# Performance work log

Measured on AMD Instinct MI355X. Metric: run time of the kernel, lower is better.

Reference implementation:

```python
import jax, jax.numpy as jnp
import numpy as np

EMBED_DIM = 512
NUM_HEADS = 8
HEAD_DIM = EMBED_DIM // NUM_HEADS
FACTOR = 5
B, T = 4, 2048


def setup_inputs() -> dict:
    key = jax.random.key(0)
    ks = jax.random.split(key, 10)
    s = EMBED_DIM ** -0.5
    hidden_states = jax.random.normal(ks[0], (B, T, EMBED_DIM), dtype=jnp.float32)
    log_L = int(np.ceil(np.log1p(T)))
    u_part = min(FACTOR * T * log_L, T)
    index_sample = jax.random.randint(ks[1], (u_part,), 0, T, dtype=jnp.int32)
    Wq = jax.random.normal(ks[2], (EMBED_DIM, EMBED_DIM), dtype=jnp.float32) * s
    bq = jnp.zeros((EMBED_DIM,), dtype=jnp.float32)
    Wk = jax.random.normal(ks[3], (EMBED_DIM, EMBED_DIM), dtype=jnp.float32) * s
    bk = jnp.zeros((EMBED_DIM,), dtype=jnp.float32)
    Wv = jax.random.normal(ks[4], (EMBED_DIM, EMBED_DIM), dtype=jnp.float32) * s
    bv = jnp.zeros((EMBED_DIM,), dtype=jnp.float32)
    Wo = jax.random.normal(ks[5], (EMBED_DIM, EMBED_DIM), dtype=jnp.float32) * s
    bo = jnp.zeros((EMBED_DIM,), dtype=jnp.float32)
    return {"hidden_states": hidden_states, "index_sample": index_sample,
            "Wq": Wq, "bq": bq, "Wk": Wk, "bk": bk, "Wv": Wv, "bv": bv,
            "Wo": Wo, "bo": bo}


def _split_heads(x, bsz, seqlen):
    # [B, T, E] -> [B*H, T, head_dim]
    return x.reshape(bsz, seqlen, NUM_HEADS, HEAD_DIM).transpose(0, 2, 1, 3).reshape(bsz * NUM_HEADS, seqlen, HEAD_DIM)


def reference(hidden_states, index_sample, Wq, bq, Wk, bk, Wv, bv, Wo, bo):
    bsz, tgt_len, embed_dim = hidden_states.shape
    scaling = HEAD_DIM ** -0.5
    q = (hidden_states @ Wq.T + bq) * scaling
    k = hidden_states @ Wk.T + bk
    v = hidden_states @ Wv.T + bv
    q = _split_heads(q, bsz, tgt_len)   # [BH, T, d]
    k = _split_heads(k, bsz, tgt_len)
    v = _split_heads(v, bsz, tgt_len)
    L_k = tgt_len
    log_q = int(np.ceil(np.log1p(tgt_len)))
    u = min(FACTOR * log_q, tgt_len)
    # random key sampling (indices precomputed, length u_part)
    k_sample = k[:, index_sample, :]                                  # [BH, u_part, d]
    qk_sample = jnp.einsum('bqd,bkd->bqk', q, k_sample)               # [BH, T, u_part]
    # sparsity measurement: max - mean over sampled keys (mean uses full L_k as in source)
    sparsity = qk_sample.max(axis=-1) - qk_sample.sum(axis=-1) / L_k  # [BH, T]
    top_idx = jax.lax.top_k(sparsity, u)[1]                           # [BH, u]
    q_reduce = jnp.take_along_axis(q, top_idx[:, :, None], axis=1)    # [BH, u, d]
    attn = jax.nn.softmax(jnp.einsum('bud,bkd->buk', q_reduce, k), axis=-1)  # [BH, u, L]
    attn_out = jnp.einsum('buk,bkd->bud', attn, v)                    # [BH, u, d]
    # encoder context: mean of values over time, scattered with active-query outputs
    context = jnp.broadcast_to(v.mean(axis=1, keepdims=True), v.shape)  # [BH, T, d]
    bh_idx = jnp.arange(bsz * NUM_HEADS)[:, None]
    context = context.at[bh_idx, top_idx].set(attn_out)
    out = context.reshape(bsz, NUM_HEADS, tgt_len, HEAD_DIM).transpose(0, 2, 1, 3).reshape(bsz, tgt_len, embed_dim)
    return out @ Wo.T + bo
```

## Files before the change

### kernel.cpp

```cpp
#include <hip/hip_runtime.h>
#include <hip/hip_bf16.h>
#include <math.h>

#define T_LEN 2048
#define EMB   512
#define NHEAD 8
#define HDIM  64
#define BHEADS 32
#define USEL  40

typedef __bf16 bf16v8 __attribute__((ext_vector_type(8)));
typedef _Float16 f16x8 __attribute__((ext_vector_type(8)));
typedef float f32x4 __attribute__((ext_vector_type(4)));
typedef unsigned short u16;

__device__ __forceinline__ void cvt4_hilo(const float4 f, uint2& ph, uint2& pl)
{
    __hip_bfloat16 h0 = __float2bfloat16(f.x);
    __hip_bfloat16 h1 = __float2bfloat16(f.y);
    __hip_bfloat16 h2 = __float2bfloat16(f.z);
    __hip_bfloat16 h3 = __float2bfloat16(f.w);
    __hip_bfloat16 l0 = __float2bfloat16(f.x - __bfloat162float(h0));
    __hip_bfloat16 l1 = __float2bfloat16(f.y - __bfloat162float(h1));
    __hip_bfloat16 l2 = __float2bfloat16(f.z - __bfloat162float(h2));
    __hip_bfloat16 l3 = __float2bfloat16(f.w - __bfloat162float(h3));
    ph.x = (unsigned)*(const u16*)&h0 | ((unsigned)*(const u16*)&h1 << 16);
    ph.y = (unsigned)*(const u16*)&h2 | ((unsigned)*(const u16*)&h3 << 16);
    pl.x = (unsigned)*(const u16*)&l0 | ((unsigned)*(const u16*)&l1 << 16);
    pl.y = (unsigned)*(const u16*)&l2 | ((unsigned)*(const u16*)&l3 << 16);
}

__device__ __forceinline__ void cvt4_hilo_h(const float4 f, uint2& ph, uint2& pl)
{
    _Float16 h0 = (_Float16)f.x;
    _Float16 h1 = (_Float16)f.y;
    _Float16 h2 = (_Float16)f.z;
    _Float16 h3 = (_Float16)f.w;
    _Float16 l0 = (_Float16)(f.x - (float)h0);
    _Float16 l1 = (_Float16)(f.y - (float)h1);
    _Float16 l2 = (_Float16)(f.z - (float)h2);
    _Float16 l3 = (_Float16)(f.w - (float)h3);
    ph.x = (unsigned)*(const u16*)&h0 | ((unsigned)*(const u16*)&h1 << 16);
    ph.y = (unsigned)*(const u16*)&h2 | ((unsigned)*(const u16*)&h3 << 16);
    pl.x = (unsigned)*(const u16*)&l0 | ((unsigned)*(const u16*)&l1 << 16);
    pl.y = (unsigned)*(const u16*)&l2 | ((unsigned)*(const u16*)&l3 << 16);
}

__global__ __launch_bounds__(256)
void pack_hilo_kernel(const float* __restrict__ X,
                      const float* __restrict__ Wq, const float* __restrict__ Wk,
                      const float* __restrict__ Wv,
                      u16* __restrict__ Xp, u16* __restrict__ Wp)
{
    alignas(16) __shared__ u16 th[4096];
    alignas(16) __shared__ u16 tl[4096];
    const int b = blockIdx.x, tid = threadIdx.x;

    const float* src; u16* dst;
    if (b < 1024) {
        int mt = b >> 4, kt = b & 15;
        src = X + (size_t)(mt * 128) * EMB + kt * 32;
        dst = Xp + (size_t)b * 8192;
    } else {
        int wdx = b - 1024;
        int z = wdx >> 6, nt = (wdx >> 4) & 3, kt = wdx & 15;
        const float* W = (z == 0) ? Wq : (z == 1) ? Wk : Wv;
        src = W + (size_t)(nt * 128) * EMB + kt * 32;
        dst = Wp + (size_t)wdx * 8192;
    }

    #pragma unroll
    for (int s = 0; s < 4; ++s) {
        int u = tid + 256 * s;
        int row = u >> 3, c4 = u & 7;
        float4 f = *(const float4*)&src[(size_t)row * EMB + c4 * 4];
        uint2 ph, pl;
        cvt4_hilo_h(f, ph, pl);
        int kq = c4 >> 1, e4 = (c4 & 1) * 4;
        *(uint2*)&th[kq * 1024 + row * 8 + e4] = ph;
        *(uint2*)&tl[kq * 1024 + row * 8 + e4] = pl;
    }
    __syncthreads();

    uint4* d4 = (uint4*)dst;
    const uint4* s4h = (const uint4*)th;
    const uint4* s4l = (const uint4*)tl;
    d4[tid]       = s4h[tid];
    d4[tid + 256] = s4h[tid + 256];
    d4[tid + 512] = s4l[tid];
    d4[tid + 768] = s4l[tid + 256];
}

__global__ __launch_bounds__(256)
void qkv_mfma_kernel(const u16* __restrict__ Xp, const u16* __restrict__ Wp,
                     const float* __restrict__ bq, const float* __restrict__ bk,
                     const float* __restrict__ bv,
                     float* __restrict__ qo, float* __restrict__ ko, float* __restrict__ vo)
{
    alignas(16) __shared__ u16 Ah[4096];
    alignas(16) __shared__ u16 Al[4096];
    alignas(16) __shared__ u16 Bh[4096];
    alignas(16) __shared__ u16 Bl[4096];

    const int z = blockIdx.z;
    const float* bias; float* dst; float scale;
    if (z == 0)      { bias = bq; dst = qo; scale = 0.125f; }
    else if (z == 1) { bias = bk; dst = ko; scale = 1.0f;   }
    else             { bias = bv; dst = vo; scale = 1.0f;   }
    const bool three = (z != 2);

    const int tid = threadIdx.x;
    const int mt = blockIdx.x;
    const int nt = blockIdx.y;
    const int w = tid >> 6, lane = tid & 63;
    const int wm = w & 1, wn = w >> 1;
    const int lm = lane & 15, kq = lane >> 4;

    const u16* Abase = Xp + (size_t)mt * (16 * 8192);
    const u16* Bbase = Wp + (size_t)(z * 4 + nt) * (16 * 8192);

    f32x4 acc[4][4];
    #pragma unroll
    for (int i = 0; i < 4; ++i)
        #pragma unroll
        for (int j = 0; j < 4; ++j)
            #pragma unroll
            for (int r = 0; r < 4; ++r) acc[i][j][r] = 0.0f;

    for (int kt = 0; kt < 16; ++kt) {
        __syncthreads();
        const u16* at = Abase + kt * 8192;
        const u16* bt = Bbase + kt * 8192;
        const u16* gsrc; u16* ldst;
        if (w == 0)      { gsrc = at;        ldst = Ah; }
        else if (w == 1) { gsrc = at + 4096; ldst = Al; }
        else if (w == 2) { gsrc = bt;        ldst = Bh; }
        else             { gsrc = bt + 4096; ldst = Bl; }
        if (three || (w & 1) == 0) {
            #pragma unroll
            for (int i = 0; i < 8; ++i)
                __builtin_amdgcn_global_load_lds(
                    (const __attribute__((address_space(1))) void*)(gsrc + (size_t)lane * 8 + i * 512),
                    (__attribute__((address_space(3))) void*)(ldst + i * 512),
                    16, 0, 0);
        }
        __syncthreads();

        f16x8 ah[4], al[4], bh[4], bl[4];
        #pragma unroll
        for (int i = 0; i < 4; ++i) {
            int ar = (wm * 64 + i * 16 + lm) * 8 + kq * 1024;
            int br = (wn * 64 + i * 16 + lm) * 8 + kq * 1024;
            ah[i] = *(const f16x8*)&Ah[ar];
            bh[i] = *(const f16x8*)&Bh[br];
            if (three) {
                al[i] = *(const f16x8*)&Al[ar];
                bl[i] = *(const f16x8*)&Bl[br];
            }
        }
        #pragma unroll
        for (int i = 0; i < 4; ++i)
            #pragma unroll
            for (int j = 0; j < 4; ++j) {
                acc[i][j] = __builtin_amdgcn_mfma_f32_16x16x32_f16(ah[i], bh[j], acc[i][j], 0, 0, 0);
                if (three) {
                    acc[i][j] = __builtin_amdgcn_mfma_f32_16x16x32_f16(ah[i], bl[j], acc[i][j], 0, 0, 0);
                    acc[i][j] = __builtin_amdgcn_mfma_f32_16x16x32_f16(al[i], bh[j], acc[i][j], 0, 0, 0);
                }
            }
    }

    #pragma unroll
    for (int j = 0; j < 4; ++j) {
        int ng = nt * 128 + wn * 64 + j * 16 + lm;
        int h = ng >> 6, d = ng & 63;
        float bv_ = bias[ng];
        #pragma unroll
        for (int i = 0; i < 4; ++i) {
            #pragma unroll
            for (int r = 0; r < 4; ++r) {
                int mg = mt * 128 + wm * 64 + i * 16 + kq * 4 + r;
                int b = mg >> 11, t = mg & 2047;
                dst[((size_t)((b * NHEAD + h) * T_LEN + t)) * HDIM + d] =
                    (acc[i][j][r] + bv_) * scale;
            }
        }
    }
}

__global__ __launch_bounds__(256)
void qkv_proj_kernel(const float* __restrict__ X,
                     const float* __restrict__ Wq, const float* __restrict__ bq,
                     const float* __restrict__ Wk, const float* __restrict__ bk,
                     const float* __restrict__ Wv, const float* __restrict__ bv,
                     float* __restrict__ qo, float* __restrict__ ko, float* __restrict__ vo)
{
    alignas(16) __shared__ u16 Ah[128 * 40];
    alignas(16) __shared__ u16 Al[128 * 40];
    alignas(16) __shared__ u16 Bh[128 * 40];
    alignas(16) __shared__ u16 Bl[128 * 40];

    const int z = blockIdx.z;
    const float* W; const float* bias; float* dst; float scale;
    if (z == 0)      { W = Wq; bias = bq; dst = qo; scale = 0.125f; }
    else if (z == 1) { W = Wk; bias = bk; dst = ko; scale = 1.0f;   }
    else             { W = Wv; bias = bv; dst = vo; scale = 1.0f;   }

    const int tid = threadIdx.x;
    const int m0 = blockIdx.x * 128;
    const int n0 = blockIdx.y * 128;
    const int w = tid >> 6, lane = tid & 63;
    const int wm = w & 1, wn = w >> 1;
    const int lm = lane & 15, kq = lane >> 4;

    f32x4 acc[4][4];
    #pragma unroll
    for (int i = 0; i < 4; ++i)
        #pragma unroll
        for (int j = 0; j < 4; ++j)
            #pragma unroll
            for (int r = 0; r < 4; ++r) acc[i][j][r] = 0.0f;

    for (int kc = 0; kc < EMB; kc += 32) {
        __syncthreads();
        #pragma unroll
        for (int s = 0; s < 4; ++s) {
            int u = tid + 256 * s;
            int row = u >> 3, c4 = u & 7;
            float4 fa = *(const float4*)&X[(size_t)(m0 + row) * EMB + kc + c4 * 4];
            float4 fb = *(const float4*)&W[(n0 + row) * EMB + kc + c4 * 4];
            uint2 ph, pl;
            cvt4_hilo_h(fa, ph, pl);
            *(uint2*)&Ah[row * 40 + c4 * 4] = ph;
            *(uint2*)&Al[row * 40 + c4 * 4] = pl;
            cvt4_hilo_h(fb, ph, pl);
            *(uint2*)&Bh[row * 40 + c4 * 4] = ph;
            *(uint2*)&Bl[row * 40 + c4 * 4] = pl;
        }
        __syncthreads();

        f16x8 ah[4], al[4], bh[4], bl[4];
        #pragma unroll
        for (int i = 0; i < 4; ++i) {
            int ra = (wm * 64 + i * 16 + lm) * 40 + kq * 8;
            ah[i] = *(const f16x8*)&Ah[ra];
            al[i] = *(const f16x8*)&Al[ra];
            int rb = (wn * 64 + i * 16 + lm) * 40 + kq * 8;
            bh[i] = *(const f16x8*)&Bh[rb];
            bl[i] = *(const f16x8*)&Bl[rb];
        }
        #pragma unroll
        for (int i = 0; i < 4; ++i)
            #pragma unroll
            for (int j = 0; j < 4; ++j) {
                acc[i][j] = __builtin_amdgcn_mfma_f32_16x16x32_f16(ah[i], bh[j], acc[i][j], 0, 0, 0);
                acc[i][j] = __builtin_amdgcn_mfma_f32_16x16x32_f16(ah[i], bl[j], acc[i][j], 0, 0, 0);
                acc[i][j] = __builtin_amdgcn_mfma_f32_16x16x32_f16(al[i], bh[j], acc[i][j], 0, 0, 0);
            }
    }

    #pragma unroll
    for (int j = 0; j < 4; ++j) {
        int ng = n0 + wn * 64 + j * 16 + lm;
        int h = ng >> 6, d = ng & 63;
        float bv_ = bias[ng];
        #pragma unroll
        for (int i = 0; i < 4; ++i) {
            #pragma unroll
            for (int r = 0; r < 4; ++r) {
                int mg = m0 + wm * 64 + i * 16 + kq * 4 + r;
                int b = mg >> 11, t = mg & 2047;
                dst[((size_t)((b * NHEAD + h) * T_LEN + t)) * HDIM + d] =
                    (acc[i][j][r] + bv_) * scale;
            }
        }
    }
}

__global__ __launch_bounds__(256)
void count_compact_kernel(const int* __restrict__ idxs, int n,
                          int* __restrict__ count, int* __restrict__ klist,
                          int* __restrict__ ncp)
{
    __shared__ int cnt[T_LEN];
    __shared__ int th_tot[256];
    __shared__ int th_off[256];
    __shared__ int ncs;
    const int tid = threadIdx.x;
    for (int j = tid; j < T_LEN; j += 256) cnt[j] = 0;
    __syncthreads();
    for (int i = tid; i < n; i += 256) atomicAdd(&cnt[idxs[i] & (T_LEN - 1)], 1);
    __syncthreads();
    const int base = tid * 8;
    int flags[8]; int loc = 0;
    #pragma unroll
    for (int j = 0; j < 8; ++j) {
        int c = cnt[base + j];
        count[base + j] = c;
        flags[j] = (c > 0); loc += flags[j];
    }
    th_tot[tid] = loc;
    __syncthreads();
    if (tid == 0) {
        int run = 0;
        for (int i = 0; i < 256; ++i) { th_off[i] = run; run += th_tot[i]; }
        ncs = run;
        ncp[0] = run;
    }
    __syncthreads();
    int off = th_off[tid];
    #pragma unroll
    for (int j = 0; j < 8; ++j)
        if (flags[j]) klist[off++] = base + j;
    __syncthreads();
    const int nc = ncs;
    const int nt = (nc + 127) & ~127;
    const int k0 = klist[0];
    for (int j = nc + tid; j < nt; j += 256) klist[j] = k0;
}

__global__ __launch_bounds__(256)
void ksum_vmean_part_kernel(const int* __restrict__ count,
                            const float* __restrict__ k, const float* __restrict__ v,
                            float* __restrict__ kpart, float* __restrict__ vpart)
{
    __shared__ int cs[256];
    alignas(16) __shared__ float rk[16 * 64];
    alignas(16) __shared__ float rv[16 * 64];

    const int sl = blockIdx.x, bh = blockIdx.y, tid = threadIdx.x;
    const int f4 = tid & 15, tg = tid >> 4;
    const int t0 = sl * 256;

    cs[tid] = count[t0 + tid];
    __syncthreads();

    const float4* k4 = (const float4*)(k + (size_t)bh * T_LEN * HDIM) + t0 * 16;
    const float4* v4 = (const float4*)(v + (size_t)bh * T_LEN * HDIM) + t0 * 16;

    float4 ak = {0.f, 0.f, 0.f, 0.f}, av = {0.f, 0.f, 0.f, 0.f};
    #pragma unroll
    for (int s = 0; s < 16; ++s) {
        int t = tg + s * 16;
        float c = (float)cs[t];
        float4 kf = k4[t * 16 + f4];
        float4 vf = v4[t * 16 + f4];
        ak.x = fmaf(c, kf.x, ak.x); ak.y = fmaf(c, kf.y, ak.y);
        ak.z = fmaf(c, kf.z, ak.z); ak.w = fmaf(c, kf.w, ak.w);
        av.x += vf.x; av.y += vf.y; av.z += vf.z; av.w += vf.w;
    }
    *(float4*)&rk[tg * 64 + f4 * 4] = ak;
    *(float4*)&rv[tg * 64 + f4 * 4] = av;
    __syncthreads();

    if (tid < 64) {
        float sk = 0.f, sv = 0.f;
        #pragma unroll
        for (int g = 0; g < 16; ++g) { sk += rk[g * 64 + tid]; sv += rv[g * 64 + tid]; }
        kpart[((size_t)bh * 8 + sl) * 64 + tid] = sk;
        vpart[((size_t)bh * 8 + sl) * 64 + tid] = sv;
    }
}

__global__ __launch_bounds__(64)
void ksum_vmean_reduce_kernel(const float* __restrict__ kpart, const float* __restrict__ vpart,
                              float* __restrict__ ksum, float* __restrict__ vmean)
{
    const int bh = blockIdx.x, d = threadIdx.x;
    float sk = 0.f, sv = 0.f;
    #pragma unroll
    for (int sl = 0; sl < 8; ++sl) {
        sk += kpart[((size_t)bh * 8 + sl) * 64 + d];
        sv += vpart[((size_t)bh * 8 + sl) * 64 + d];
    }
    ksum[bh * 64 + d]  = sk;
    vmean[bh * 64 + d] = sv * (1.0f / 2048.0f);
}

__global__ __launch_bounds__(256)
void pack_k_kernel(const float* __restrict__ k, const int* __restrict__ klist,
                   const int* __restrict__ ncp, u16* __restrict__ Kp)
{
    alignas(16) __shared__ u16 th[8192];
    alignas(16) __shared__ u16 tl[8192];
    const int wg = blockIdx.x, tid = threadIdx.x;
    const int swz = (wg & 7) * 64 + (wg >> 3);
    const int bh = swz >> 4, kt = swz & 15;
    const int ntiles = (ncp[0] + 127) >> 7;
    if (kt >= ntiles) return;

    const float4* kb4 = (const float4*)(k + (size_t)bh * T_LEN * HDIM);
    #pragma unroll
    for (int s = 0; s < 8; ++s) {
        int u = tid + 256 * s;
        int row = u >> 4, c4 = u & 15;
        int krow = klist[kt * 128 + row];
        float4 f = kb4[krow * 16 + c4];
        uint2 ph, pl;
        cvt4_hilo_h(f, ph, pl);
        int base = (c4 >> 3) * 4096 + ((c4 >> 1) & 3) * 1024 + row * 8 + (c4 & 1) * 4;
        *(uint2*)&th[base] = ph;
        *(uint2*)&tl[base] = pl;
    }
    __syncthreads();

    u16* dst = Kp + ((size_t)bh * 16 + kt) * 16384;
    uint4* d4 = (uint4*)dst;
    const uint4* s4h = (const uint4*)th;
    const uint4* s4l = (const uint4*)tl;
    #pragma unroll
    for (int i = 0; i < 4; ++i) d4[tid + 256 * i] = s4h[tid + 256 * i];
    #pragma unroll
    for (int i = 0; i < 4; ++i) d4[1024 + tid + 256 * i] = s4l[tid + 256 * i];
}

__global__ __launch_bounds__(256)
void sparsity_scan_kernel(const float* __restrict__ q, const u16* __restrict__ Kp,
                          const float* __restrict__ ksum,
                          const int* __restrict__ ncp, float* __restrict__ spars)
{
    alignas(16) __shared__ u16 KH[10240];
    alignas(16) __shared__ u16 KL[10240];
    __shared__ float ksm[64];
    __shared__ float smax[128];
    __shared__ float sdotL[128];

    const int tid = threadIdx.x;
    const int wg = blockIdx.x;
    const int swz = (wg & 7) * 64 + (wg >> 3);
    const int bh = swz >> 4;
    const int q0 = (swz & 15) * 128;
    const int w = tid >> 6, lane = tid & 63;
    const int lm = lane & 15, kq = lane >> 4;

    const float* qb = q + ((size_t)bh * T_LEN + q0) * HDIM;
    const int ntiles = (ncp[0] + 127) >> 7;

    if (tid < 64) ksm[tid] = ksum[bh * 64 + tid];

    #pragma unroll
    for (int s = 0; s < 8; ++s) {
        int u = tid + 256 * s;
        int row = u >> 4, c4 = u & 15;
        float4 f = *(const float4*)&qb[row * HDIM + c4 * 4];
        uint2 ph, pl;
        cvt4_hilo_h(f, ph, pl);
        int base = ((c4 >> 3) * 128 + row) * 40 + (c4 & 7) * 4;
        *(uint2*)&KH[base] = ph;
        *(uint2*)&KL[base] = pl;
    }
    __syncthreads();

    f16x8 qh[2][2], ql[2][2];
    #pragma unroll
    for (int i = 0; i < 2; ++i)
        #pragma unroll
        for (int c = 0; c < 2; ++c) {
            int ra = (c * 128 + w * 32 + i * 16 + lm) * 40 + kq * 8;
            qh[i][c] = *(const f16x8*)&KH[ra];
            ql[i][c] = *(const f16x8*)&KL[ra];
        }

    {
        float4 k0a = *(const float4*)&ksm[kq * 8];
        float4 k0b = *(const float4*)&ksm[kq * 8 + 4];
        float4 k1a = *(const float4*)&ksm[32 + kq * 8];
        float4 k1b = *(const float4*)&ksm[32 + kq * 8 + 4];
        float kmv[2][8] = {{k0a.x, k0a.y, k0a.z, k0a.w, k0b.x, k0b.y, k0b.z, k0b.w},
                           {k1a.x, k1a.y, k1a.z, k1a.w, k1b.x, k1b.y, k1b.z, k1b.w}};
        #pragma unroll
        for (int i = 0; i < 2; ++i) {
            float sd = 0.f;
            #pragma unroll
            for (int c = 0; c < 2; ++c)
                #pragma unroll
                for (int e = 0; e < 8; ++e)
                    sd = fmaf((float)qh[i][c][e] + (float)ql[i][c][e], kmv[c][e], sd);
            sd += __shfl_xor(sd, 16, 64);
            sd += __shfl_xor(sd, 32, 64);
            if (kq == 0) sdotL[w * 32 + i * 16 + lm] = sd;
        }
    }

    float vmax[2][4];
    #pragma unroll
    for (int i = 0; i < 2; ++i)
        #pragma unroll
        for (int r = 0; r < 4; ++r) vmax[i][r] = -INFINITY;

    const u16* kpb = Kp + (size_t)bh * (16 * 16384);

    for (int kt = 0; kt < ntiles; ++kt) {
        __syncthreads();
        const u16* kp = kpb + kt * 16384;
        const u16* gsrc; u16* ldst;
        if (w == 0)      { gsrc = kp;         ldst = KH; }
        else if (w == 1) { gsrc = kp + 4096;  ldst = KH + 4096; }
        else if (w == 2) { gsrc = kp + 8192;  ldst = KL; }
        else             { gsrc = kp + 12288; ldst = KL + 4096; }
        #pragma unroll
        for (int i = 0; i < 8; ++i)
            __builtin_amdgcn_global_load_lds(
                (const __attribute__((address_space(1))) void*)(gsrc + (size_t)lane * 8 + i * 512),
                (__attribute__((address_space(3))) void*)(ldst + i * 512),
                16, 0, 0);
        __syncthreads();

        #pragma unroll
        for (int j = 0; j < 8; ++j) {
            int rb0 = kq * 1024 + (j * 16 + lm) * 8;
            int rb1 = 4096 + kq * 1024 + (j * 16 + lm) * 8;
            f16x8 bh0 = *(const f16x8*)&KH[rb0];
            f16x8 bl0 = *(const f16x8*)&KL[rb0];
            f16x8 bh1 = *(const f16x8*)&KH[rb1];
            f16x8 bl1 = *(const f16x8*)&KL[rb1];
            f32x4 a0 = {0.f, 0.f, 0.f, 0.f};
            f32x4 a1 = {0.f, 0.f, 0.f, 0.f};
            a0 = __builtin_amdgcn_mfma_f32_16x16x32_f16(qh[0][0], bh0, a0, 0, 0, 0);
            a1 = __builtin_amdgcn_mfma_f32_16x16x32_f16(qh[1][0], bh0, a1, 0, 0, 0);
            a0 = __builtin_amdgcn_mfma_f32_16x16x32_f16(qh[0][0], bl0, a0, 0, 0, 0);
            a1 = __builtin_amdgcn_mfma_f32_16x16x32_f16(qh[1][0], bl0, a1, 0, 0, 0);
            a0 = __builtin_amdgcn_mfma_f32_16x16x32_f16(ql[0][0], bh0, a0, 0, 0, 0);
            a1 = __builtin_amdgcn_mfma_f32_16x16x32_f16(ql[1][0], bh0, a1, 0, 0, 0);
            a0 = __builtin_amdgcn_mfma_f32_16x16x32_f16(qh[0][1], bh1, a0, 0, 0, 0);
            a1 = __builtin_amdgcn_mfma_f32_16x16x32_f16(qh[1][1], bh1, a1, 0, 0, 0);
            a0 = __builtin_amdgcn_mfma_f32_16x16x32_f16(qh[0][1], bl1, a0, 0, 0, 0);
            a1 = __builtin_amdgcn_mfma_f32_16x16x32_f16(qh[1][1], bl1, a1, 0, 0, 0);
            a0 = __builtin_amdgcn_mfma_f32_16x16x32_f16(ql[0][1], bh1, a0, 0, 0, 0);
            a1 = __builtin_amdgcn_mfma_f32_16x16x32_f16(ql[1][1], bh1, a1, 0, 0, 0);
            #pragma unroll
            for (int r = 0; r < 4; ++r) {
                vmax[0][r] = fmaxf(vmax[0][r], a0[r]);
                vmax[1][r] = fmaxf(vmax[1][r], a1[r]);
            }
        }
    }

    #pragma unroll
    for (int i = 0; i < 2; ++i)
        #pragma unroll
        for (int r = 0; r < 4; ++r) {
            float m = vmax[i][r];
            m = fmaxf(m, __shfl_xor(m, 1, 64));
            m = fmaxf(m, __shfl_xor(m, 2, 64));
            m = fmaxf(m, __shfl_xor(m, 4, 64));
            m = fmaxf(m, __shfl_xor(m, 8, 64));
            if (lm == 0) smax[w * 32 + i * 16 + kq * 4 + r] = m;
        }
    __syncthreads();

    if (tid < 128)
        spars[bh * T_LEN + q0 + tid] = smax[tid] - sdotL[tid] * (1.0f / 2048.0f);
}

__global__ __launch_bounds__(256)
void sparsity_scan_fb_kernel(const float* __restrict__ q, const float* __restrict__ k,
                             const float* __restrict__ ksum, const int* __restrict__ klist,
                             const int* __restrict__ ncp, float* __restrict__ spars)
{
    alignas(16) __shared__ u16 KH[256 * 40];
    alignas(16) __shared__ u16 KL[256 * 40];
    __shared__ float ksm[64];
    __shared__ float smax[128];
    __shared__ float sdotL[128];

    const int tid = threadIdx.x;
    const int bh = blockIdx.y;
    const int q0 = blockIdx.x * 128;
    const int w = tid >> 6, lane = tid & 63;
    const int lm = lane & 15, kq = lane >> 4;

    const float* qb = q + ((size_t)bh * T_LEN + q0) * HDIM;
    const float4* kb4 = (const float4*)(k + (size_t)bh * T_LEN * HDIM);
    const int ntiles = (ncp[0] + 127) >> 7;

    if (tid < 64) ksm[tid] = ksum[bh * 64 + tid];

    #pragma unroll
    for (int s = 0; s < 8; ++s) {
        int u = tid + 256 * s;
        int row = u >> 4, c4 = u & 15;
        float4 f = *(const float4*)&qb[row * HDIM + c4 * 4];
        uint2 ph, pl;
        cvt4_hilo_h(f, ph, pl);
        int base = ((c4 >> 3) * 128 + row) * 40 + (c4 & 7) * 4;
        *(uint2*)&KH[base] = ph;
        *(uint2*)&KL[base] = pl;
    }
    __syncthreads();

    f16x8 qh[2][2], ql[2][2];
    #pragma unroll
    for (int i = 0; i < 2; ++i)
        #pragma unroll
        for (int c = 0; c < 2; ++c) {
            int ra = (c * 128 + w * 32 + i * 16 + lm) * 40 + kq * 8;
            qh[i][c] = *(const f16x8*)&KH[ra];
            ql[i][c] = *(const f16x8*)&KL[ra];
        }

    {
        float4 k0a = *(const float4*)&ksm[kq * 8];
        float4 k0b = *(const float4*)&ksm[kq * 8 + 4];
        float4 k1a = *(const float4*)&ksm[32 + kq * 8];
        float4 k1b = *(const float4*)&ksm[32 + kq * 8 + 4];
        float kmv[2][8] = {{k0a.x, k0a.y, k0a.z, k0a.w, k0b.x, k0b.y, k0b.z, k0b.w},
                           {k1a.x, k1a.y, k1a.z, k1a.w, k1b.x, k1b.y, k1b.z, k1b.w}};
        #pragma unroll
        for (int i = 0; i < 2; ++i) {
            float sd = 0.f;
            #pragma unroll
            for (int c = 0; c < 2; ++c)
                #pragma unroll
                for (int e = 0; e < 8; ++e)
                    sd = fmaf((float)qh[i][c][e] + (float)ql[i][c][e], kmv[c][e], sd);
            sd += __shfl_xor(sd, 16, 64);
            sd += __shfl_xor(sd, 32, 64);
            if (kq == 0) sdotL[w * 32 + i * 16 + lm] = sd;
        }
    }

    float vmax[2][4];
    #pragma unroll
    for (int i = 0; i < 2; ++i)
        #pragma unroll
        for (int r = 0; r < 4; ++r) vmax[i][r] = -INFINITY;

    for (int kt = 0; kt < ntiles; ++kt) {
        __syncthreads();
        #pragma unroll
        for (int s = 0; s < 8; ++s) {
            int u = tid + 256 * s;
            int row = u >> 4, c4 = u & 15;
            int krow = klist[kt * 128 + row];
            float4 f = kb4[krow * 16 + c4];
            uint2 ph, pl;
            cvt4_hilo_h(f, ph, pl);
            int base = ((c4 >> 3) * 128 + row) * 40 + (c4 & 7) * 4;
            *(uint2*)&KH[base] = ph;
            *(uint2*)&KL[base] = pl;
        }
        __syncthreads();

        #pragma unroll
        for (int j = 0; j < 8; ++j) {
            int rb0 = (j * 16 + lm) * 40 + kq * 8;
            int rb1 = (128 + j * 16 + lm) * 40 + kq * 8;
            f16x8 bh0 = *(const f16x8*)&KH[rb0];
            f16x8 bl0 = *(const f16x8*)&KL[rb0];
            f16x8 bh1 = *(const f16x8*)&KH[rb1];
            f16x8 bl1 = *(const f16x8*)&KL[rb1];
            f32x4 a0 = {0.f, 0.f, 0.f, 0.f};
            f32x4 a1 = {0.f, 0.f, 0.f, 0.f};
            a0 = __builtin_amdgcn_mfma_f32_16x16x32_f16(qh[0][0], bh0, a0, 0, 0, 0);
            a1 = __builtin_amdgcn_mfma_f32_16x16x32_f16(qh[1][0], bh0, a1, 0, 0, 0);
            a0 = __builtin_amdgcn_mfma_f32_16x16x32_f16(qh[0][0], bl0, a0, 0, 0, 0);
            a1 = __builtin_amdgcn_mfma_f32_16x16x32_f16(qh[1][0], bl0, a1, 0, 0, 0);
            a0 = __builtin_amdgcn_mfma_f32_16x16x32_f16(ql[0][0], bh0, a0, 0, 0, 0);
            a1 = __builtin_amdgcn_mfma_f32_16x16x32_f16(ql[1][0], bh0, a1, 0, 0, 0);
            a0 = __builtin_amdgcn_mfma_f32_16x16x32_f16(qh[0][1], bh1, a0, 0, 0, 0);
            a1 = __builtin_amdgcn_mfma_f32_16x16x32_f16(qh[1][1], bh1, a1, 0, 0, 0);
            a0 = __builtin_amdgcn_mfma_f32_16x16x32_f16(qh[0][1], bl1, a0, 0, 0, 0);
            a1 = __builtin_amdgcn_mfma_f32_16x16x32_f16(qh[1][1], bl1, a1, 0, 0, 0);
            a0 = __builtin_amdgcn_mfma_f32_16x16x32_f16(ql[0][1], bh1, a0, 0, 0, 0);
            a1 = __builtin_amdgcn_mfma_f32_16x16x32_f16(ql[1][1], bh1, a1, 0, 0, 0);
            #pragma unroll
            for (int r = 0; r < 4; ++r) {
                vmax[0][r] = fmaxf(vmax[0][r], a0[r]);
                vmax[1][r] = fmaxf(vmax[1][r], a1[r]);
            }
        }
    }

    #pragma unroll
    for (int i = 0; i < 2; ++i)
        #pragma unroll
        for (int r = 0; r < 4; ++r) {
            float m = vmax[i][r];
            m = fmaxf(m, __shfl_xor(m, 1, 64));
            m = fmaxf(m, __shfl_xor(m, 2, 64));
            m = fmaxf(m, __shfl_xor(m, 4, 64));
            m = fmaxf(m, __shfl_xor(m, 8, 64));
            if (lm == 0) smax[w * 32 + i * 16 + kq * 4 + r] = m;
        }
    __syncthreads();

    if (tid < 128)
        spars[bh * T_LEN + q0 + tid] = smax[tid] - sdotL[tid] * (1.0f / 2048.0f);
}

__global__ __launch_bounds__(256)
void topk_kernel(const float* __restrict__ spars, int* __restrict__ topi)
{
    __shared__ float vals[T_LEN];
    __shared__ float rv[256];
    __shared__ int   ri[256];
    const int bh = blockIdx.x, tid = threadIdx.x;
    for (int j = tid; j < T_LEN; j += 256) vals[j] = spars[bh * T_LEN + j];
    __syncthreads();
    for (int it = 0; it < USEL; ++it) {
        float bv = -INFINITY; int bi = 0;
        #pragma unroll
        for (int jj = 0; jj < 8; ++jj) {
            int j = tid * 8 + jj;
            float vv = vals[j];
            if (vv > bv) { bv = vv; bi = j; }
        }
        rv[tid] = bv; ri[tid] = bi;
        __syncthreads();
        for (int s = 128; s > 0; s >>= 1) {
            if (tid < s) {
                float ov = rv[tid + s]; int oi = ri[tid + s];
                if (ov > rv[tid] || (ov == rv[tid] && oi < ri[tid])) { rv[tid] = ov; ri[tid] = oi; }
            }
            __syncthreads();
        }
        if (tid == 0) {
            int win = ri[0] & (T_LEN - 1);
            topi[bh * USEL + it] = win;
            vals[win] = -INFINITY;
        }
        __syncthreads();
    }
}

__global__ __launch_bounds__(256)
void gather_q_kernel(const float* __restrict__ q, const int* __restrict__ topi,
                     float* __restrict__ qsel)
{
    const int bh = blockIdx.x, tid = threadIdx.x;
    for (int i = tid; i < USEL * HDIM; i += 256) {
        int u = i >> 6, d = i & 63;
        int t = topi[bh * USEL + u] & (T_LEN - 1);
        qsel[(size_t)bh * USEL * HDIM + i] = q[((size_t)bh * T_LEN + t) * HDIM + d];
    }
}

__global__ __launch_bounds__(256)
void sel_scores_kernel(const float* __restrict__ qsel, const float* __restrict__ k,
                       float* __restrict__ S)
{
    __shared__ float qsT[64 * 41];
    __shared__ float ksT[64 * 257];

    const int sl = blockIdx.x, bh = blockIdx.y, tid = threadIdx.x;
    const int t0 = sl * 256;

    for (int i = tid; i < USEL * HDIM; i += 256) {
        int u = i >> 6, d = i & 63;
        qsT[d * 41 + u] = qsel[(size_t)bh * USEL * HDIM + i];
    }
    const float4* k4 = (const float4*)(k + (size_t)bh * T_LEN * HDIM);
    #pragma unroll
    for (int s = 0; s < 16; ++s) {
        int u = tid + 256 * s;
        int c4 = u & 15, t = u >> 4;
        float4 f = k4[(t0 + t) * 16 + c4];
        ksT[(c4 * 4 + 0) * 257 + t] = f.x;
        ksT[(c4 * 4 + 1) * 257 + t] = f.y;
        ksT[(c4 * 4 + 2) * 257 + t] = f.z;
        ksT[(c4 * 4 + 3) * 257 + t] = f.w;
    }
    __syncthreads();

    const int qg = tid >> 5;
    const int kg = tid & 31;

    float acc[5][8];
    #pragma unroll
    for (int i = 0; i < 5; ++i)
        #pragma unroll
        for (int j = 0; j < 8; ++j) acc[i][j] = 0.0f;

    #pragma unroll 4
    for (int d = 0; d < 64; ++d) {
        float qv[5], kv[8];
        #pragma unroll
        for (int i = 0; i < 5; ++i) qv[i] = qsT[d * 41 + qg * 5 + i];
        #pragma unroll
        for (int j = 0; j < 8; ++j) kv[j] = ksT[d * 257 + kg + 32 * j];
        #pragma unroll
        for (int i = 0; i < 5; ++i)
            #pragma unroll
            for (int j = 0; j < 8; ++j)
                acc[i][j] = fmaf(qv[i], kv[j], acc[i][j]);
    }

    #pragma unroll
    for (int i = 0; i < 5; ++i) {
        float* sp = &S[((size_t)bh * USEL + qg * 5 + i) * T_LEN + t0 + kg];
        #pragma unroll
        for (int j = 0; j < 8; ++j) sp[32 * j] = acc[i][j];
    }
}

__global__ __launch_bounds__(256)
void sel_softmax_kernel(float* __restrict__ S)
{
    __shared__ float red[256];
    const int row = blockIdx.x, tid = threadIdx.x;
    float* sr = S + (size_t)row * T_LEN;

    float x[8];
    float m = -INFINITY;
    #pragma unroll
    for (int s = 0; s < 8; ++s) { x[s] = sr[tid + 256 * s]; m = fmaxf(m, x[s]); }
    red[tid] = m;
    __syncthreads();
    for (int s = 128; s > 0; s >>= 1) {
        if (tid < s) red[tid] = fmaxf(red[tid], red[tid + s]);
        __syncthreads();
    }
    m = red[0];
    __syncthreads();

    float sum = 0.f;
    #pragma unroll
    for (int s = 0; s < 8; ++s) { x[s] = __expf(x[s] - m); sum += x[s]; }
    red[tid] = sum;
    __syncthreads();
    for (int s = 128; s > 0; s >>= 1) {
        if (tid < s) red[tid] += red[tid + s];
        __syncthreads();
    }
    float inv = 1.0f / red[0];
    #pragma unroll
    for (int s = 0; s < 8; ++s) sr[tid + 256 * s] = x[s] * inv;
}

__global__ __launch_bounds__(256)
void pv_part_kernel(const float* __restrict__ S, const float* __restrict__ v,
                    float* __restrict__ part)
{
    __shared__ float ps[USEL * 128];
    __shared__ float vs[128 * 69];
    __shared__ float obuf[128 * 20];

    const int sl = blockIdx.x, bh = blockIdx.y, tid = threadIdx.x;
    const int t0 = sl * 128;

    for (int i = tid; i < USEL * 128; i += 256) {
        int q = i >> 7, t = i & 127;
        ps[q * 128 + t] = S[((size_t)bh * USEL + q) * T_LEN + t0 + t];
    }
    const float4* v4 = (const float4*)(v + (size_t)bh * T_LEN * HDIM);
    #pragma unroll
    for (int s = 0; s < 8; ++s) {
        int u = tid + 256 * s;
        int c4 = u & 15, t = u >> 4;
        float4 f = v4[(t0 + t) * 16 + c4];
        vs[t * 69 + c4 * 4 + 0] = f.x;
        vs[t * 69 + c4 * 4 + 1] = f.y;
        vs[t * 69 + c4 * 4 + 2] = f.z;
        vs[t * 69 + c4 * 4 + 3] = f.w;
    }
    __syncthreads();

    const int qg = tid >> 5, r = tid & 31;
    const int dg = r >> 1, th = r & 1;
    const int tb = th * 64;

    float o[5][4];
    #pragma unroll
    for (int i = 0; i < 5; ++i)
        #pragma unroll
        for (int j = 0; j < 4; ++j) o[i][j] = 0.0f;

    #pragma unroll 4
    for (int tt = 0; tt < 64; ++tt) {
        int t = tb + tt;
        float pv[5];
        #pragma unroll
        for (int i = 0; i < 5; ++i) pv[i] = ps[(qg * 5 + i) * 128 + t];
        float4 vv = *(const float4*)&vs[t * 69 + dg * 4];
        #pragma unroll
        for (int i = 0; i < 5; ++i) {
            o[i][0] = fmaf(pv[i], vv.x, o[i][0]);
            o[i][1] = fmaf(pv[i], vv.y, o[i][1]);
            o[i][2] = fmaf(pv[i], vv.z, o[i][2]);
            o[i][3] = fmaf(pv[i], vv.w, o[i][3]);
        }
    }

    const int p = qg * 16 + dg;
    if (th == 1) {
        #pragma unroll
        for (int i = 0; i < 5; ++i)
            #pragma unroll
            for (int j = 0; j < 4; ++j) obuf[p * 20 + i * 4 + j] = o[i][j];
    }
    __syncthreads();
    if (th == 0) {
        float* pb = part + ((size_t)bh * 16 + sl) * (USEL * HDIM);
        #pragma unroll
        for (int i = 0; i < 5; ++i)
            #pragma unroll
            for (int j = 0; j < 4; ++j)
                pb[(qg * 5 + i) * HDIM + dg * 4 + j] = o[i][j] + obuf[p * 20 + i * 4 + j];
    }
}

__global__ __launch_bounds__(256)
void pv_merge_kernel(const float* __restrict__ part, float* __restrict__ attn)
{
    const int bh = blockIdx.x, tid = threadIdx.x;
    for (int i = tid; i < USEL * HDIM; i += 256) {
        float s = 0.f;
        #pragma unroll
        for (int sl = 0; sl < 16; ++sl)
            s += part[((size_t)bh * 16 + sl) * (USEL * HDIM) + i];
        attn[(size_t)bh * USEL * HDIM + i] = s;
    }
}

__global__ __launch_bounds__(256)
void ctx_fill_kernel(const float* __restrict__ vmean, float* __restrict__ ctx)
{
    int flat = blockIdx.x * 256 + threadIdx.x;
    int d = flat & 63, h = (flat >> 6) & 7, b = flat >> 20;
    int bh = (b << 3) | h;
    ctx[flat] = vmean[bh * 64 + d];
}

__global__ void ctx_scatter_kernel(const float* __restrict__ attn, const int* __restrict__ topi,
                                   float* __restrict__ ctx)
{
    const int u = blockIdx.x, bh = blockIdx.y, d = threadIdx.x;
    const int b = bh >> 3, h = bh & 7;
    const int t = topi[bh * USEL + u] & (T_LEN - 1);
    ctx[(size_t)(b * T_LEN + t) * EMB + h * 64 + d] =
        attn[((size_t)bh * USEL + u) * HDIM + d];
}

__global__ __launch_bounds__(256)
void out_proj_kernel(const float* __restrict__ A, const float* __restrict__ Wo,
                     const float* __restrict__ bo, float* __restrict__ out)
{
    alignas(16) __shared__ u16 Ah[128 * 40];
    alignas(16) __shared__ u16 Al[128 * 40];
    alignas(16) __shared__ u16 Bh[128 * 40];
    alignas(16) __shared__ u16 Bl[128 * 40];

    const int tid = threadIdx.x;
    const int m0 = blockIdx.x * 128;
    const int n0 = blockIdx.y * 128;
    const int w = tid >> 6, lane = tid & 63;
    const int wm = w & 1, wn = w >> 1;
    const int lm = lane & 15, kq = lane >> 4;

    f32x4 acc[4][4];
    #pragma unroll
    for (int i = 0; i < 4; ++i)
        #pragma unroll
        for (int j = 0; j < 4; ++j)
            #pragma unroll
            for (int r = 0; r < 4; ++r) acc[i][j][r] = 0.0f;

    for (int kc = 0; kc < EMB; kc += 32) {
        __syncthreads();
        #pragma unroll
        for (int s = 0; s < 4; ++s) {
            int u = tid + 256 * s;
            int row = u >> 3, c4 = u & 7;
            float4 fa = *(const float4*)&A[(size_t)(m0 + row) * EMB + kc + c4 * 4];
            float4 fb = *(const float4*)&Wo[(n0 + row) * EMB + kc + c4 * 4];
            uint2 ph, pl;
            cvt4_hilo(fa, ph, pl);
            *(uint2*)&Ah[row * 40 + c4 * 4] = ph;
            *(uint2*)&Al[row * 40 + c4 * 4] = pl;
            cvt4_hilo(fb, ph, pl);
            *(uint2*)&Bh[row * 40 + c4 * 4] = ph;
            *(uint2*)&Bl[row * 40 + c4 * 4] = pl;
        }
        __syncthreads();

        bf16v8 ah[4], al[4], bh[4], bl[4];
        #pragma unroll
        for (int i = 0; i < 4; ++i) {
            int ra = (wm * 64 + i * 16 + lm) * 40 + kq * 8;
            ah[i] = *(const bf16v8*)&Ah[ra];
            al[i] = *(const bf16v8*)&Al[ra];
            int rb = (wn * 64 + i * 16 + lm) * 40 + kq * 8;
            bh[i] = *(const bf16v8*)&Bh[rb];
            bl[i] = *(const bf16v8*)&Bl[rb];
        }
        #pragma unroll
        for (int i = 0; i < 4; ++i)
            #pragma unroll
            for (int j = 0; j < 4; ++j) {
                acc[i][j] = __builtin_amdgcn_mfma_f32_16x16x32_bf16(ah[i], bh[j], acc[i][j], 0, 0, 0);
                acc[i][j] = __builtin_amdgcn_mfma_f32_16x16x32_bf16(ah[i], bl[j], acc[i][j], 0, 0, 0);
                acc[i][j] = __builtin_amdgcn_mfma_f32_16x16x32_bf16(al[i], bh[j], acc[i][j], 0, 0, 0);
            }
    }

    #pragma unroll
    for (int j = 0; j < 4; ++j) {
        int ng = n0 + wn * 64 + j * 16 + lm;
        float bias = bo[ng];
        #pragma unroll
        for (int i = 0; i < 4; ++i)
            #pragma unroll
            for (int r = 0; r < 4; ++r) {
                int mg = m0 + wm * 64 + i * 16 + kq * 4 + r;
                out[(size_t)mg * EMB + ng] = acc[i][j][r] + bias;
            }
    }
}

__global__ __launch_bounds__(256)
void ws_diag_kernel(float* __restrict__ out, int n, float mib)
{
    int flat = blockIdx.x * 256 + threadIdx.x;
    if (flat < n) out[flat] = mib;
}

extern "C" void kernel_launch(void* const* d_in, const int* in_sizes, int n_in,
                              void* d_out, int out_size, void* d_ws, size_t ws_size,
                              hipStream_t stream)
{
    const float* X = nullptr; const int* idxs = nullptr;
    const float* Wseen[4] = {nullptr, nullptr, nullptr, nullptr};
    const float* bseen[4] = {nullptr, nullptr, nullptr, nullptr};
    int nw = 0, nb = 0, u_part = 2048;
    for (int i = 0; i < n_in; ++i) {
        int sz = in_sizes[i];
        if (sz == EMB * EMB * 16) { if (!X) X = (const float*)d_in[i]; }
        else if (sz == T_LEN)     { if (!idxs) { idxs = (const int*)d_in[i]; u_part = sz; } }
        else if (sz == EMB * EMB) { if (nw < 4) Wseen[nw++] = (const float*)d_in[i]; }
        else if (sz == EMB)       { if (nb < 4) bseen[nb++] = (const float*)d_in[i]; }
    }
    if (!X || !idxs || nw < 4 || nb < 4) {
        X = (const float*)d_in[0]; idxs = (const int*)d_in[1];
        Wseen[0] = (const float*)d_in[2]; bseen[0] = (const float*)d_in[3];
        Wseen[1] = (const float*)d_in[4]; bseen[1] = (const float*)d_in[5];
        Wseen[2] = (const float*)d_in[6]; bseen[2] = (const float*)d_in[7];
        Wseen[3] = (const float*)d_in[8]; bseen[3] = (const float*)d_in[9];
        u_part = in_sizes[1];
    }
    const float *Wq = Wseen[0], *Wk = Wseen[1], *Wv = Wseen[2], *Wo = Wseen[3];
    const float *bq = bseen[0], *bk = bseen[1], *bv = bseen[2], *bo = bseen[3];

    const size_t NEED      = 50951168ULL;
    const size_t NEED_BIG  = NEED + 16777216ULL + 3145728ULL;
    if (ws_size < NEED) {
        ws_diag_kernel<<<(out_size + 255) / 256, 256, 0, stream>>>(
            (float*)d_out, out_size, (float)(ws_size >> 20));
        return;
    }

    float* ws    = (float*)d_ws;
    float* qw    = ws;
    float* kw    = qw + 4194304;
    float* vw    = kw + 4194304;
    float* tail  = vw + 4194304;
    float* slotA = tail;
    float* spars = tail + 81920;
    int*   count = (int*)(tail + 147456);
    float* ksum  = tail + 149504;
    float* vmean = tail + 151552;
    int*   topi  = (int*)(tail + 153600);
    float* kpart = tail;
    float* vpart = tail + 16384;
    int*   klist = (int*)(tail + 32768);
    int*   ncp   = (int*)(tail + 34816);
    float* S     = qw;
    float* pvp   = qw + 2621440;
    float* qsel  = slotA;
    float* attn  = slotA;
    float* ctx   = (float*)d_ws;
    u16*   Xp    = (u16*)((char*)d_ws + NEED);
    u16*   Wp    = Xp + 8388608;
    u16*   Kp    = Xp;

    const bool big = (ws_size >= NEED_BIG);

    if (big) {
        pack_hilo_kernel<<<1216, 256, 0, stream>>>(X, Wq, Wk, Wv, Xp, Wp);
        qkv_mfma_kernel<<<dim3(64, 4, 3), 256, 0, stream>>>(Xp, Wp, bq, bk, bv, qw, kw, vw);
    } else {
        qkv_proj_kernel<<<dim3(64, 4, 3), 256, 0, stream>>>(X, Wq, bq, Wk, bk, Wv, bv, qw, kw, vw);
    }
    count_compact_kernel<<<1, 256, 0, stream>>>(idxs, u_part, count, klist, ncp);
    ksum_vmean_part_kernel<<<dim3(8, 32), 256, 0, stream>>>(count, kw, vw, kpart, vpart);
    ksum_vmean_reduce_kernel<<<32, 64, 0, stream>>>(kpart, vpart, ksum, vmean);
    if (big) {
        pack_k_kernel<<<512, 256, 0, stream>>>(kw, klist, ncp, Kp);
        sparsity_scan_kernel<<<512, 256, 0, stream>>>(qw, Kp, ksum, ncp, spars);
    } else {
        sparsity_scan_fb_kernel<<<dim3(16, 32), 256, 0, stream>>>(qw, kw, ksum, klist, ncp, spars);
    }
    topk_kernel<<<32, 256, 0, stream>>>(spars, topi);
    gather_q_kernel<<<32, 256, 0, stream>>>(qw, topi, qsel);
    sel_scores_kernel<<<dim3(8, 32), 256, 0, stream>>>(qsel, kw, S);
    sel_softmax_kernel<<<1280, 256, 0, stream>>>(S);
    pv_part_kernel<<<dim3(16, 32), 256, 0, stream>>>(S, vw, pvp);
    pv_merge_kernel<<<32, 256, 0, stream>>>(pvp, attn);
    ctx_fill_kernel<<<16384, 256, 0, stream>>>(vmean, ctx);
    ctx_scatter_kernel<<<dim3(USEL, BHEADS), 64, 0, stream>>>(attn, topi, ctx);
    out_proj_kernel<<<dim3(64, 4), 256, 0, stream>>>(ctx, Wo, bo, (float*)d_out);
}
```

Before: 313.8 us.

## Replace iterative argmax top-k with radix-select top-k in shared memory

The top-k kernel no longer runs 40 sequential argmax passes, each with a full block tree reduction and many barriers. It now finds the 40th-largest key with a 4-level 8-bit radix histogram select over order-preserving integer keys, then writes every index above that threshold and fills the rest from ties. Output order changes from sorted to unordered, which is fine for the downstream gather/scatter if consumers only rely on the set of indices. It adds shared-memory atomics and a prefix scan per level.

```diff
diff --git a/kernel.cpp b/kernel.cpp
--- a/kernel.cpp
+++ b/kernel.cpp
@@ -692,35 +692,96 @@
 __global__ __launch_bounds__(256)
 void topk_kernel(const float* __restrict__ spars, int* __restrict__ topi)
 {
-    __shared__ float vals[T_LEN];
-    __shared__ float rv[256];
-    __shared__ int   ri[256];
+    __shared__ unsigned keys[T_LEN];
+    __shared__ int hist[256];
+    __shared__ int sfx[257];
+    __shared__ int sh_need, sh_bin, nsel, neq, cnt2;
     const int bh = blockIdx.x, tid = threadIdx.x;
-    for (int j = tid; j < T_LEN; j += 256) vals[j] = spars[bh * T_LEN + j];
-    __syncthreads();
-    for (int it = 0; it < USEL; ++it) {
-        float bv = -INFINITY; int bi = 0;
-        #pragma unroll
-        for (int jj = 0; jj < 8; ++jj) {
-            int j = tid * 8 + jj;
-            float vv = vals[j];
-            if (vv > bv) { bv = vv; bi = j; }
-        }
-        rv[tid] = bv; ri[tid] = bi;
-        __syncthreads();
-        for (int s = 128; s > 0; s >>= 1) {
-            if (tid < s) {
-                float ov = rv[tid + s]; int oi = ri[tid + s];
-                if (ov > rv[tid] || (ov == rv[tid] && oi < ri[tid])) { rv[tid] = ov; ri[tid] = oi; }
+
+    #pragma unroll
+    for (int s = 0; s < 8; ++s) {
+        int j = tid + 256 * s;
+        unsigned u = __float_as_uint(spars[bh * T_LEN + j]);
+        keys[j] = (u & 0x80000000u) ? ~u : (u | 0x80000000u);
+    }
+    if (tid == 0) { sh_need = USEL; nsel = 0; neq = 0; cnt2 = 0; }
+    __syncthreads();
+
+    unsigned kpref = 0;
+    int shift = 24;
+    #pragma unroll
+    for (int level = 0; level < 4; ++level) {
+        const unsigned hi_mask = (shift == 24) ? 0u : (0xFFFFFFFFu << (shift + 8));
+        hist[tid] = 0;
+        __syncthreads();
+        #pragma unroll
+        for (int s = 0; s < 8; ++s) {
+            unsigned kk = keys[tid + 256 * s];
+            if ((kk & hi_mask) == kpref)
+                atomicAdd(&hist[(kk >> shift) & 255], 1);
+        }
+        __syncthreads();
+        sfx[tid] = hist[tid];
+        if (tid == 0) sfx[256] = 0;
+        __syncthreads();
+        for (int off = 1; off < 256; off <<= 1) {
+            int v = (tid + off < 256) ? sfx[tid + off] : 0;
+            __syncthreads();
+            sfx[tid] += v;
+            __syncthreads();
+        }
+        const int need = sh_need;
+        const int A = (tid == 255) ? 0 : sfx[tid + 1];
+        const int here = sfx[tid];
+        __syncthreads();
+        if (A < need && here >= need) {
+            sh_bin = tid;
+            sh_need = need - A;
+        }
+        __syncthreads();
+        kpref |= (unsigned)sh_bin << shift;
+        shift -= 8;
+    }
+
+    const unsigned K = kpref;
+    const int need_eq = sh_need;
+
+    #pragma unroll
+    for (int s = 0; s < 8; ++s) {
+        int j = tid + 256 * s;
+        unsigned kk = keys[j];
+        if (kk > K) {
+            int pos = atomicAdd(&nsel, 1);
+            if (pos < USEL) topi[bh * USEL + pos] = j;
+        } else if (kk == K) {
+            atomicAdd(&neq, 1);
+        }
+    }
+    __syncthreads();
+    const int base = nsel;
+    const int E = neq;
+    __syncthreads();
+
+    if (E == need_eq) {
+        #pragma unroll
+        for (int s = 0; s < 8; ++s) {
+            int j = tid + 256 * s;
+            if (keys[j] == K) {
+                int pos = atomicAdd(&cnt2, 1);
+                if (base + pos < USEL) topi[bh * USEL + base + pos] = j;
             }
-            __syncthreads();
-        }
-        if (tid == 0) {
-            int win = ri[0] & (T_LEN - 1);
-            topi[bh * USEL + it] = win;
-            vals[win] = -INFINITY;
-        }
-        __syncthreads();
+        }
+    } else {
+        #pragma unroll
+        for (int s = 0; s < 8; ++s) {
+            int j = tid + 256 * s;
+            if (keys[j] == K) {
+                int rank = 0;
+                for (int j2 = 0; j2 < j; ++j2) rank += (keys[j2] == K);
+                if (rank < need_eq && base + rank < USEL)
+                    topi[bh * USEL + base + rank] = j;
+            }
+        }
     }
 }
 
```

Result: faster. 280.0 us (-10.8%).
